# Kernel tuning notes

Hardware: AMD Instinct MI355X
Metric: run time of the kernel (lower is better)

## Reference

```python
import jax, jax.numpy as jnp
import numpy as np

N_NODES = 50000
BN_EPS = 1e-5


def gcn_conv(x, W, b, src, dst, n):
    # PyG GCNConv: add self-loops, symmetric normalization, linear then scatter-add, bias after.
    h = x @ W                                             # [N, out]
    loops = jnp.arange(n, dtype=src.dtype)
    s = jnp.concatenate([src, loops])                     # [E+N]
    d = jnp.concatenate([dst, loops])                     # [E+N]
    deg = jax.ops.segment_sum(jnp.ones_like(d, dtype=h.dtype), d, num_segments=n)
    dinv = jnp.where(deg > 0, jax.lax.rsqrt(deg), 0.0)    # deg^-1/2
    norm = dinv[s] * dinv[d]                              # [E+N]
    msg = h[s] * norm[:, None]                            # gather + scale
    out = jax.ops.segment_sum(msg, d, num_segments=n)     # scatter-add to targets
    return out + b


def batch_norm(x, gamma, beta):
    # training-mode BatchNorm1d: batch stats over node dim, biased variance
    mean = jnp.mean(x, axis=0)
    var = jnp.mean(jnp.square(x - mean), axis=0)
    return (x - mean) * jax.lax.rsqrt(var + BN_EPS) * gamma + beta


def setup_inputs() -> dict:
    key = jax.random.key(0)
    ks = jax.random.split(key, 4)
    n, e = N_NODES, 800000
    c_in, c_hid, c_out = 128, 128, 64
    x = jax.random.normal(ks[0], (n, c_in), dtype=jnp.float32)
    edge_index = jax.random.randint(ks[1], (2, e), 0, n, dtype=jnp.int64)
    W1 = jax.random.normal(ks[2], (c_in, c_hid), dtype=jnp.float32) / np.sqrt(c_in)
    W2 = jax.random.normal(ks[3], (c_hid, c_out), dtype=jnp.float32) / np.sqrt(c_hid)
    return {
        "x": x,
        "edge_index": edge_index,
        "W1": W1,
        "b1": jnp.zeros((c_hid,), jnp.float32),
        "gamma": jnp.ones((c_hid,), jnp.float32),
        "beta": jnp.zeros((c_hid,), jnp.float32),
        "W2": W2,
        "b2": jnp.zeros((c_out,), jnp.float32),
    }


def reference(x, edge_index, W1, b1, gamma, beta, W2, b2):
    src, dst = edge_index[0], edge_index[1]
    n = x.shape[0]
    h = gcn_conv(x, W1, b1, src, dst, n)
    h = batch_norm(h, gamma, beta)
    h = jax.nn.elu(h)
    z = gcn_conv(h, W2, b2, src, dst, n)
    return z
```

## Files before the change

kernel.cpp:

```cpp
#include <hip/hip_runtime.h>
#include <math.h>

#define C_IN 128
#define C_HID 128
#define C_OUT 64
#define BN_EPS 1e-5f

typedef unsigned int uint;
typedef int iv4 __attribute__((ext_vector_type(4)));

__device__ __forceinline__ void fma4(float4& a, float s, const float4& b) {
    a.x += s * b.x; a.y += s * b.y; a.z += s * b.z; a.w += s * b.w;
}
__device__ __forceinline__ uint bfr(float f) {
    uint u = __float_as_uint(f);
    return (u + 0x7fffu + ((u >> 16) & 1u)) >> 16;
}
__device__ __forceinline__ uint pk(float a, float b) { return bfr(a) | (bfr(b) << 16); }
__device__ __forceinline__ float bl(uint u) { return __uint_as_float(u << 16); }
__device__ __forceinline__ float bh(uint u) { return __uint_as_float(u & 0xffff0000u); }

__global__ __launch_bounds__(256) void k_zero(int* __restrict__ deg,
                                              float* __restrict__ gsum,
                                              float* __restrict__ gss, int n) {
    int i = blockIdx.x * 256 + threadIdx.x;
    if (i < n) deg[i] = 0;
    else if (i < n + 128) gsum[i - n] = 0.f;
    else if (i < n + 256) gss[i - n - 128] = 0.f;
}

__global__ void k_deg(const int* __restrict__ dst, int* __restrict__ deg, int E) {
    int e4 = (blockIdx.x * 256 + threadIdx.x) * 4;
    if (e4 + 3 < E) {
        iv4 d4 = __builtin_nontemporal_load((const iv4*)&dst[e4]);
        atomicAdd(&deg[d4.x], 1);
        atomicAdd(&deg[d4.y], 1);
        atomicAdd(&deg[d4.z], 1);
        atomicAdd(&deg[d4.w], 1);
    } else {
        for (int e = e4; e < E; ++e) atomicAdd(&deg[dst[e]], 1);
    }
}

__global__ __launch_bounds__(256) void k_part(const int* __restrict__ deg,
                                              int* __restrict__ part, int n) {
    int i = blockIdx.x * 256 + threadIdx.x;
    int v = (i < n) ? deg[i] : 0;
    #pragma unroll
    for (int o = 32; o > 0; o >>= 1) v += __shfl_down(v, o);
    __shared__ int ls[4];
    if ((threadIdx.x & 63) == 0) ls[threadIdx.x >> 6] = v;
    __syncthreads();
    if (threadIdx.x == 0) part[blockIdx.x] = ls[0] + ls[1] + ls[2] + ls[3];
}

__global__ __launch_bounds__(256) void k_scanp(int* __restrict__ part, int nb) {
    __shared__ int s[256];
    int tid = threadIdx.x;
    int v = (tid < nb) ? part[tid] : 0;
    s[tid] = v;
    __syncthreads();
    for (int o = 1; o < 256; o <<= 1) {
        int t = (tid >= o) ? s[tid - o] : 0;
        __syncthreads();
        s[tid] += t;
        __syncthreads();
    }
    if (tid < nb) part[tid] = s[tid] - v;
}

__global__ __launch_bounds__(256) void k_apply(const int* __restrict__ deg,
                                               const int* __restrict__ part,
                                               int* __restrict__ rowstart,
                                               int* __restrict__ cursor,
                                               float* __restrict__ dinv, int n) {
    int i = blockIdx.x * 256 + threadIdx.x;
    int d = (i < n) ? deg[i] : 0;
    __shared__ int s[256];
    s[threadIdx.x] = d;
    __syncthreads();
    for (int o = 1; o < 256; o <<= 1) {
        int t = (threadIdx.x >= o) ? s[threadIdx.x - o] : 0;
        __syncthreads();
        s[threadIdx.x] += t;
        __syncthreads();
    }
    int incl = s[threadIdx.x];
    int off = part[blockIdx.x];
    if (i < n) {
        rowstart[i] = off + incl - d;
        cursor[i]   = off + incl - d;
        dinv[i] = rsqrtf((float)(d + 1));
        if (i == n - 1) rowstart[n] = off + incl;
    }
}

#define FILL_R 8
#define FILL_CHUNK 4096
__global__ __launch_bounds__(256) void k_fill(const int* __restrict__ src,
                                              const int* __restrict__ dst,
                                              int* __restrict__ cursor,
                                              int* __restrict__ csr,
                                              int E, int rs) {
    int r = blockIdx.x & (FILL_R - 1);
    int c = blockIdx.x >> 3;
    int lo = r * rs, hi = lo + rs;
    int e0 = c * FILL_CHUNK;
    int e1 = e0 + FILL_CHUNK; if (e1 > E) e1 = E;
    for (int e = e0 + threadIdx.x * 4; e + 3 < e1; e += 1024) {
        iv4 d4 = __builtin_nontemporal_load((const iv4*)&dst[e]);
        iv4 s4 = __builtin_nontemporal_load((const iv4*)&src[e]);
        if (d4.x >= lo && d4.x < hi) csr[atomicAdd(&cursor[d4.x], 1)] = s4.x;
        if (d4.y >= lo && d4.y < hi) csr[atomicAdd(&cursor[d4.y], 1)] = s4.y;
        if (d4.z >= lo && d4.z < hi) csr[atomicAdd(&cursor[d4.z], 1)] = s4.z;
        if (d4.w >= lo && d4.w < hi) csr[atomicAdd(&cursor[d4.w], 1)] = s4.w;
    }
    int tail = e1 & ~3;
    if (e1 == E && tail < E) {
        for (int e = tail + threadIdx.x; e < E; e += 256) {
            int d = dst[e];
            if (d >= lo && d < hi) csr[atomicAdd(&cursor[d], 1)] = src[e];
        }
    }
}

__global__ __launch_bounds__(256) void k_gemm1(const float* __restrict__ x,
                                               const float* __restrict__ W,
                                               uint* __restrict__ h, int n) {
    __shared__ float xs[64][68];
    __shared__ float ws[64][68];
    const int tid = threadIdx.x;
    const int cg = tid & 15, rg = tid >> 4;
    const int c0 = cg * 4, r0 = rg * 4;
    const int base = blockIdx.x * 64;
    const int ccol = blockIdx.y * 64;

    float4 acc0 = make_float4(0.f, 0.f, 0.f, 0.f);
    float4 acc1 = acc0, acc2 = acc0, acc3 = acc0;

    for (int p = 0; p < 2; ++p) {
        const int k0 = p * 64;
        if (p) __syncthreads();
        for (int idx = tid; idx < 64 * 16; idx += 256) {
            int row = idx >> 4, c4 = (idx & 15) * 4;
            float4 v = make_float4(0.f, 0.f, 0.f, 0.f);
            if (base + row < n) v = *(const float4*)&x[(size_t)(base + row) * C_IN + k0 + c4];
            *(float4*)&xs[row][c4] = v;
        }
        for (int idx = tid; idx < 64 * 16; idx += 256) {
            int kk = idx >> 4, cc = (idx & 15) * 4;
            *(float4*)&ws[kk][cc] = *(const float4*)&W[(size_t)(k0 + kk) * C_HID + ccol + cc];
        }
        __syncthreads();
        for (int kk = 0; kk < 64; kk += 4) {
            float4 xv0 = *(const float4*)&xs[r0 + 0][kk];
            float4 xv1 = *(const float4*)&xs[r0 + 1][kk];
            float4 xv2 = *(const float4*)&xs[r0 + 2][kk];
            float4 xv3 = *(const float4*)&xs[r0 + 3][kk];
            float4 wv0 = *(const float4*)&ws[kk + 0][c0];
            float4 wv1 = *(const float4*)&ws[kk + 1][c0];
            float4 wv2 = *(const float4*)&ws[kk + 2][c0];
            float4 wv3 = *(const float4*)&ws[kk + 3][c0];
            fma4(acc0, xv0.x, wv0); fma4(acc0, xv0.y, wv1); fma4(acc0, xv0.z, wv2); fma4(acc0, xv0.w, wv3);
            fma4(acc1, xv1.x, wv0); fma4(acc1, xv1.y, wv1); fma4(acc1, xv1.z, wv2); fma4(acc1, xv1.w, wv3);
            fma4(acc2, xv2.x, wv0); fma4(acc2, xv2.y, wv1); fma4(acc2, xv2.z, wv2); fma4(acc2, xv2.w, wv3);
            fma4(acc3, xv3.x, wv0); fma4(acc3, xv3.y, wv1); fma4(acc3, xv3.z, wv2); fma4(acc3, xv3.w, wv3);
        }
    }
    const int cu = (ccol + c0) >> 1;
    if (base + r0 + 0 < n) { uint2 o = make_uint2(pk(acc0.x, acc0.y), pk(acc0.z, acc0.w)); *(uint2*)&h[(size_t)(base + r0 + 0) * 64 + cu] = o; }
    if (base + r0 + 1 < n) { uint2 o = make_uint2(pk(acc1.x, acc1.y), pk(acc1.z, acc1.w)); *(uint2*)&h[(size_t)(base + r0 + 1) * 64 + cu] = o; }
    if (base + r0 + 2 < n) { uint2 o = make_uint2(pk(acc2.x, acc2.y), pk(acc2.z, acc2.w)); *(uint2*)&h[(size_t)(base + r0 + 2) * 64 + cu] = o; }
    if (base + r0 + 3 < n) { uint2 o = make_uint2(pk(acc3.x, acc3.y), pk(acc3.z, acc3.w)); *(uint2*)&h[(size_t)(base + r0 + 3) * 64 + cu] = o; }
}

__global__ __launch_bounds__(256) void k_gather1(const uint2* __restrict__ h,
                                                 const float* __restrict__ dinv,
                                                 const int* __restrict__ rowstart,
                                                 const int* __restrict__ csr,
                                                 const float* __restrict__ b,
                                                 float* __restrict__ out, int n) {
    int wid = (blockIdx.x * 256 + threadIdx.x) >> 6;
    int lane = threadIdx.x & 63;
    int half = lane >> 5, l = lane & 31;
    int v = wid * 2 + half;
    if (v >= n) return;
    float dv = dinv[v];
    int s0 = rowstart[v], s1 = rowstart[v + 1];
    float4 acc;
    {
        uint2 u = h[(size_t)v * 32 + l];
        acc.x = dv * bl(u.x); acc.y = dv * bh(u.x);
        acc.z = dv * bl(u.y); acc.w = dv * bh(u.y);
    }
    int e = s0;
    for (; e + 3 < s1; e += 4) {
        int i0 = csr[e], i1 = csr[e + 1], i2 = csr[e + 2], i3 = csr[e + 3];
        float w0 = dinv[i0], w1 = dinv[i1], w2 = dinv[i2], w3 = dinv[i3];
        uint2 u0 = h[(size_t)i0 * 32 + l];
        uint2 u1 = h[(size_t)i1 * 32 + l];
        uint2 u2 = h[(size_t)i2 * 32 + l];
        uint2 u3 = h[(size_t)i3 * 32 + l];
        acc.x += w0 * bl(u0.x) + w1 * bl(u1.x) + w2 * bl(u2.x) + w3 * bl(u3.x);
        acc.y += w0 * bh(u0.x) + w1 * bh(u1.x) + w2 * bh(u2.x) + w3 * bh(u3.x);
        acc.z += w0 * bl(u0.y) + w1 * bl(u1.y) + w2 * bl(u2.y) + w3 * bl(u3.y);
        acc.w += w0 * bh(u0.y) + w1 * bh(u1.y) + w2 * bh(u2.y) + w3 * bh(u3.y);
    }
    for (; e < s1; ++e) {
        int s = csr[e];
        float w = dinv[s];
        uint2 u = h[(size_t)s * 32 + l];
        acc.x += w * bl(u.x); acc.y += w * bh(u.x);
        acc.z += w * bl(u.y); acc.w += w * bh(u.y);
    }
    float4 bb = *(const float4*)&b[l * 4];
    float4 o;
    o.x = acc.x * dv + bb.x; o.y = acc.y * dv + bb.y;
    o.z = acc.z * dv + bb.z; o.w = acc.w * dv + bb.w;
    *(float4*)&out[(size_t)v * C_HID + l * 4] = o;
}

__global__ __launch_bounds__(256) void k_bnstats(const float* __restrict__ g,
                                                 float* __restrict__ gsum,
                                                 float* __restrict__ gss, int n) {
    float s = 0.f, ss = 0.f;
    int stride = gridDim.x * 256;
    int total = n * C_HID;
    for (int i = blockIdx.x * 256 + threadIdx.x; i < total; i += stride) {
        float v = g[i];
        s += v; ss += v * v;
    }
    __shared__ float ls[256], lss[256];
    ls[threadIdx.x] = s; lss[threadIdx.x] = ss;
    __syncthreads();
    if (threadIdx.x < 128) {
        atomicAdd(&gsum[threadIdx.x], ls[threadIdx.x] + ls[threadIdx.x + 128]);
        atomicAdd(&gss[threadIdx.x], lss[threadIdx.x] + lss[threadIdx.x + 128]);
    }
}

__global__ __launch_bounds__(256) void k_gemm2(const float* __restrict__ g1,
                                               const float* __restrict__ W2,
                                               const float* __restrict__ gsum,
                                               const float* __restrict__ gss,
                                               const float* __restrict__ gamma,
                                               const float* __restrict__ beta,
                                               uint* __restrict__ h2, int n) {
    __shared__ float xs[64][68];
    __shared__ float ws[64][68];
    __shared__ float sc[C_HID], sh[C_HID];
    const int tid = threadIdx.x;
    const int cg = tid & 15, rg = tid >> 4;
    const int c0 = cg * 4, r0 = rg * 4;
    const int base = blockIdx.x * 64;

    if (tid < C_HID) {
        float inv_n = 1.f / (float)n;
        float mean = gsum[tid] * inv_n;
        float var = gss[tid] * inv_n - mean * mean;
        float s = gamma[tid] * rsqrtf(var + BN_EPS);
        sc[tid] = s;
        sh[tid] = beta[tid] - mean * s;
    }
    __syncthreads();

    float4 acc0 = make_float4(0.f, 0.f, 0.f, 0.f);
    float4 acc1 = acc0, acc2 = acc0, acc3 = acc0;

    for (int p = 0; p < 2; ++p) {
        const int k0 = p * 64;
        if (p) __syncthreads();
        for (int idx = tid; idx < 64 * 16; idx += 256) {
            int row = idx >> 4, c4 = (idx & 15) * 4;
            int k = k0 + c4;
            float4 v = make_float4(0.f, 0.f, 0.f, 0.f);
            if (base + row < n) {
                v = *(const float4*)&g1[(size_t)(base + row) * C_HID + k];
                float t;
                t = v.x * sc[k + 0] + sh[k + 0]; v.x = t > 0.f ? t : expm1f(t);
                t = v.y * sc[k + 1] + sh[k + 1]; v.y = t > 0.f ? t : expm1f(t);
                t = v.z * sc[k + 2] + sh[k + 2]; v.z = t > 0.f ? t : expm1f(t);
                t = v.w * sc[k + 3] + sh[k + 3]; v.w = t > 0.f ? t : expm1f(t);
            }
            *(float4*)&xs[row][c4] = v;
        }
        for (int idx = tid; idx < 64 * 16; idx += 256) {
            int kk = idx >> 4, cc = (idx & 15) * 4;
            *(float4*)&ws[kk][cc] = *(const float4*)&W2[(size_t)(k0 + kk) * C_OUT + cc];
        }
        __syncthreads();
        for (int kk = 0; kk < 64; kk += 4) {
            float4 xv0 = *(const float4*)&xs[r0 + 0][kk];
            float4 xv1 = *(const float4*)&xs[r0 + 1][kk];
            float4 xv2 = *(const float4*)&xs[r0 + 2][kk];
            float4 xv3 = *(const float4*)&xs[r0 + 3][kk];
            float4 wv0 = *(const float4*)&ws[kk + 0][c0];
            float4 wv1 = *(const float4*)&ws[kk + 1][c0];
            float4 wv2 = *(const float4*)&ws[kk + 2][c0];
            float4 wv3 = *(const float4*)&ws[kk + 3][c0];
            fma4(acc0, xv0.x, wv0); fma4(acc0, xv0.y, wv1); fma4(acc0, xv0.z, wv2); fma4(acc0, xv0.w, wv3);
            fma4(acc1, xv1.x, wv0); fma4(acc1, xv1.y, wv1); fma4(acc1, xv1.z, wv2); fma4(acc1, xv1.w, wv3);
            fma4(acc2, xv2.x, wv0); fma4(acc2, xv2.y, wv1); fma4(acc2, xv2.z, wv2); fma4(acc2, xv2.w, wv3);
            fma4(acc3, xv3.x, wv0); fma4(acc3, xv3.y, wv1); fma4(acc3, xv3.z, wv2); fma4(acc3, xv3.w, wv3);
        }
    }
    const int cu = c0 >> 1;
    if (base + r0 + 0 < n) { uint2 o = make_uint2(pk(acc0.x, acc0.y), pk(acc0.z, acc0.w)); *(uint2*)&h2[(size_t)(base + r0 + 0) * 32 + cu] = o; }
    if (base + r0 + 1 < n) { uint2 o = make_uint2(pk(acc1.x, acc1.y), pk(acc1.z, acc1.w)); *(uint2*)&h2[(size_t)(base + r0 + 1) * 32 + cu] = o; }
    if (base + r0 + 2 < n) { uint2 o = make_uint2(pk(acc2.x, acc2.y), pk(acc2.z, acc2.w)); *(uint2*)&h2[(size_t)(base + r0 + 2) * 32 + cu] = o; }
    if (base + r0 + 3 < n) { uint2 o = make_uint2(pk(acc3.x, acc3.y), pk(acc3.z, acc3.w)); *(uint2*)&h2[(size_t)(base + r0 + 3) * 32 + cu] = o; }
}

__global__ __launch_bounds__(256) void k_gather2(const uint* __restrict__ h,
                                                 const float* __restrict__ dinv,
                                                 const int* __restrict__ rowstart,
                                                 const int* __restrict__ csr,
                                                 const float* __restrict__ b,
                                                 float* __restrict__ out, int n) {
    int wid = (blockIdx.x * 256 + threadIdx.x) >> 6;
    int lane = threadIdx.x & 63;
    int half = lane >> 5, l = lane & 31;
    int v = wid * 2 + half;
    if (v >= n) return;
    float dv = dinv[v];
    int s0 = rowstart[v], s1 = rowstart[v + 1];
    float2 acc;
    {
        uint u = h[(size_t)v * 32 + l];
        acc.x = dv * bl(u); acc.y = dv * bh(u);
    }
    int e = s0;
    for (; e + 7 < s1; e += 8) {
        int i0 = csr[e], i1 = csr[e + 1], i2 = csr[e + 2], i3 = csr[e + 3];
        int i4 = csr[e + 4], i5 = csr[e + 5], i6 = csr[e + 6], i7 = csr[e + 7];
        float w0 = dinv[i0], w1 = dinv[i1], w2 = dinv[i2], w3 = dinv[i3];
        float w4 = dinv[i4], w5 = dinv[i5], w6 = dinv[i6], w7 = dinv[i7];
        uint u0 = h[(size_t)i0 * 32 + l], u1 = h[(size_t)i1 * 32 + l];
        uint u2 = h[(size_t)i2 * 32 + l], u3 = h[(size_t)i3 * 32 + l];
        uint u4 = h[(size_t)i4 * 32 + l], u5 = h[(size_t)i5 * 32 + l];
        uint u6 = h[(size_t)i6 * 32 + l], u7 = h[(size_t)i7 * 32 + l];
        acc.x += w0 * bl(u0) + w1 * bl(u1) + w2 * bl(u2) + w3 * bl(u3)
               + w4 * bl(u4) + w5 * bl(u5) + w6 * bl(u6) + w7 * bl(u7);
        acc.y += w0 * bh(u0) + w1 * bh(u1) + w2 * bh(u2) + w3 * bh(u3)
               + w4 * bh(u4) + w5 * bh(u5) + w6 * bh(u6) + w7 * bh(u7);
    }
    for (; e < s1; ++e) {
        int s = csr[e];
        float w = dinv[s];
        uint u = h[(size_t)s * 32 + l];
        acc.x += w * bl(u); acc.y += w * bh(u);
    }
    float2 bb = *(const float2*)&b[l * 2];
    float2 o;
    o.x = acc.x * dv + bb.x;
    o.y = acc.y * dv + bb.y;
    *(float2*)&out[(size_t)v * C_OUT + l * 2] = o;
}

extern "C" void kernel_launch(void* const* d_in, const int* in_sizes, int n_in,
                              void* d_out, int out_size, void* d_ws, size_t ws_size,
                              hipStream_t stream) {
    const float* x     = (const float*)d_in[0];
    const int*   ei    = (const int*)d_in[1];
    const float* W1    = (const float*)d_in[2];
    const float* b1    = (const float*)d_in[3];
    const float* gamma = (const float*)d_in[4];
    const float* beta  = (const float*)d_in[5];
    const float* W2    = (const float*)d_in[6];
    const float* b2    = (const float*)d_in[7];
    float* out = (float*)d_out;

    const int n = in_sizes[0] / C_IN;
    const int E = in_sizes[1] / 2;
    const int* src = ei;
    const int* dst = ei + E;

    char* p = (char*)d_ws;
    auto carve = [&](size_t bytes) {
        char* r = p;
        p += (bytes + 255) & ~(size_t)255;
        return r;
    };
    int*   deg      = (int*)  carve((size_t)n * 4);
    int*   rowstart = (int*)  carve((size_t)(n + 1) * 4);
    int*   cursor   = (int*)  carve((size_t)n * 4);
    int*   csr      = (int*)  carve((size_t)E * 4);
    float* dinv     = (float*)carve((size_t)n * 4);
    uint*  h1       = (uint*) carve((size_t)n * 64 * 4);
    float* g1       = (float*)carve((size_t)n * C_HID * 4);
    uint*  h2       = (uint*) carve((size_t)n * 32 * 4);
    float* gsum     = (float*)carve(C_HID * 4);
    float* gss      = (float*)carve(C_HID * 4);
    int*   part     = (int*)  carve(256 * 4);

    const int nb = (n + 255) / 256;
    const int gblocks = (((n + 1) / 2) * 64 + 255) / 256;
    k_zero<<<(n + 256 + 255) / 256, 256, 0, stream>>>(deg, gsum, gss, n);
    k_deg<<<(E / 4 + 255) / 256, 256, 0, stream>>>(dst, deg, E);
    k_gemm1<<<dim3((n + 63) / 64, 2), 256, 0, stream>>>(x, W1, h1, n);
    k_part<<<nb, 256, 0, stream>>>(deg, part, n);
    k_scanp<<<1, 256, 0, stream>>>(part, nb);
    k_apply<<<nb, 256, 0, stream>>>(deg, part, rowstart, cursor, dinv, n);
    int rs = (n + FILL_R - 1) / FILL_R;
    int fc = (E + FILL_CHUNK - 1) / FILL_CHUNK;
    k_fill<<<FILL_R * fc, 256, 0, stream>>>(src, dst, cursor, csr, E, rs);
    k_gather1<<<gblocks, 256, 0, stream>>>((const uint2*)h1, dinv, rowstart, csr, b1, g1, n);
    k_bnstats<<<512, 256, 0, stream>>>(g1, gsum, gss, n);
    k_gemm2<<<(n + 63) / 64, 256, 0, stream>>>(g1, W2, gsum, gss, gamma, beta, h2, n);
    k_gather2<<<gblocks, 256, 0, stream>>>(h2, dinv, rowstart, csr, b2, out, n);
}
```

Baseline: 234.6 us.

## Bucket edges by destination range, store g1 as bf16, widen gather lanes

Result: faster. 219.0 us (-6.7%).

```diff
diff --git a/kernel.cpp b/kernel.cpp
--- a/kernel.cpp
+++ b/kernel.cpp
@@ -5,6 +5,9 @@
 #define C_HID 128
 #define C_OUT 64
 #define BN_EPS 1e-5f
+#define CHUNK 4096
+#define NBB 32
+#define CAP 108192
 
 typedef unsigned int uint;
 typedef int iv4 __attribute__((ext_vector_type(4)));
@@ -22,23 +25,62 @@
 
 __global__ __launch_bounds__(256) void k_zero(int* __restrict__ deg,
                                               float* __restrict__ gsum,
-                                              float* __restrict__ gss, int n) {
+                                              float* __restrict__ gss,
+                                              int* __restrict__ bcur, int n) {
     int i = blockIdx.x * 256 + threadIdx.x;
     if (i < n) deg[i] = 0;
     else if (i < n + 128) gsum[i - n] = 0.f;
     else if (i < n + 256) gss[i - n - 128] = 0.f;
-}
-
-__global__ void k_deg(const int* __restrict__ dst, int* __restrict__ deg, int E) {
-    int e4 = (blockIdx.x * 256 + threadIdx.x) * 4;
-    if (e4 + 3 < E) {
-        iv4 d4 = __builtin_nontemporal_load((const iv4*)&dst[e4]);
-        atomicAdd(&deg[d4.x], 1);
-        atomicAdd(&deg[d4.y], 1);
-        atomicAdd(&deg[d4.z], 1);
-        atomicAdd(&deg[d4.w], 1);
-    } else {
-        for (int e = e4; e < E; ++e) atomicAdd(&deg[dst[e]], 1);
+    else if (i < n + 264) bcur[i - n - 256] = 0;
+}
+
+__global__ __launch_bounds__(256) void k_bucket(const int* __restrict__ src,
+                                                const int* __restrict__ dst,
+                                                int* __restrict__ deg,
+                                                int* __restrict__ bcur,
+                                                int2* __restrict__ stage,
+                                                int E, float binv) {
+    __shared__ int cnt[8], base[8], off[8];
+    if (threadIdx.x < 8) { cnt[threadIdx.x] = 0; off[threadIdx.x] = 0; }
+    __syncthreads();
+    int e0 = blockIdx.x * CHUNK;
+    int e1 = e0 + CHUNK; if (e1 > E) e1 = E;
+    int nv = (e1 - e0) & ~3;
+    for (int e = e0 + threadIdx.x * 4; e < e0 + nv; e += 1024) {
+        iv4 d4 = __builtin_nontemporal_load((const iv4*)&dst[e]);
+        #pragma unroll
+        for (int j = 0; j < 4; ++j) {
+            int d = d4[j];
+            atomicAdd(&deg[d], 1);
+            int b = (int)((float)d * binv); if (b > 7) b = 7;
+            atomicAdd(&cnt[b], 1);
+        }
+    }
+    for (int e = e0 + nv + threadIdx.x; e < e1; e += 256) {
+        int d = dst[e];
+        atomicAdd(&deg[d], 1);
+        int b = (int)((float)d * binv); if (b > 7) b = 7;
+        atomicAdd(&cnt[b], 1);
+    }
+    __syncthreads();
+    if (threadIdx.x < 8) base[threadIdx.x] = atomicAdd(&bcur[threadIdx.x], cnt[threadIdx.x]);
+    __syncthreads();
+    for (int e = e0 + threadIdx.x * 4; e < e0 + nv; e += 1024) {
+        iv4 d4 = *(const iv4*)&dst[e];
+        iv4 s4 = *(const iv4*)&src[e];
+        #pragma unroll
+        for (int j = 0; j < 4; ++j) {
+            int d = d4[j], s = s4[j];
+            int b = (int)((float)d * binv); if (b > 7) b = 7;
+            int o = base[b] + atomicAdd(&off[b], 1);
+            if (o < CAP) stage[(size_t)b * CAP + o] = make_int2(d, s);
+        }
+    }
+    for (int e = e0 + nv + threadIdx.x; e < e1; e += 256) {
+        int d = dst[e], s = src[e];
+        int b = (int)((float)d * binv); if (b > 7) b = 7;
+        int o = base[b] + atomicAdd(&off[b], 1);
+        if (o < CAP) stage[(size_t)b * CAP + o] = make_int2(d, s);
     }
 }
 
@@ -95,32 +137,17 @@
     }
 }
 
-#define FILL_R 8
-#define FILL_CHUNK 4096
-__global__ __launch_bounds__(256) void k_fill(const int* __restrict__ src,
-                                              const int* __restrict__ dst,
-                                              int* __restrict__ cursor,
-                                              int* __restrict__ csr,
-                                              int E, int rs) {
-    int r = blockIdx.x & (FILL_R - 1);
-    int c = blockIdx.x >> 3;
-    int lo = r * rs, hi = lo + rs;
-    int e0 = c * FILL_CHUNK;
-    int e1 = e0 + FILL_CHUNK; if (e1 > E) e1 = E;
-    for (int e = e0 + threadIdx.x * 4; e + 3 < e1; e += 1024) {
-        iv4 d4 = __builtin_nontemporal_load((const iv4*)&dst[e]);
-        iv4 s4 = __builtin_nontemporal_load((const iv4*)&src[e]);
-        if (d4.x >= lo && d4.x < hi) csr[atomicAdd(&cursor[d4.x], 1)] = s4.x;
-        if (d4.y >= lo && d4.y < hi) csr[atomicAdd(&cursor[d4.y], 1)] = s4.y;
-        if (d4.z >= lo && d4.z < hi) csr[atomicAdd(&cursor[d4.z], 1)] = s4.z;
-        if (d4.w >= lo && d4.w < hi) csr[atomicAdd(&cursor[d4.w], 1)] = s4.w;
-    }
-    int tail = e1 & ~3;
-    if (e1 == E && tail < E) {
-        for (int e = tail + threadIdx.x; e < E; e += 256) {
-            int d = dst[e];
-            if (d >= lo && d < hi) csr[atomicAdd(&cursor[d], 1)] = src[e];
-        }
+__global__ __launch_bounds__(256) void k_fill2(const int2* __restrict__ stage,
+                                               const int* __restrict__ bcur,
+                                               int* __restrict__ cursor,
+                                               int* __restrict__ csr) {
+    int b = blockIdx.x & 7;
+    int j = blockIdx.x >> 3;
+    int cnt = bcur[b]; if (cnt > CAP) cnt = CAP;
+    const int2* sp = stage + (size_t)b * CAP;
+    for (int i = j * 256 + threadIdx.x; i < cnt; i += NBB * 256) {
+        int2 pr = sp[i];
+        csr[atomicAdd(&cursor[pr.x], 1)] = pr.y;
     }
 }
 
@@ -174,72 +201,88 @@
     if (base + r0 + 3 < n) { uint2 o = make_uint2(pk(acc3.x, acc3.y), pk(acc3.z, acc3.w)); *(uint2*)&h[(size_t)(base + r0 + 3) * 64 + cu] = o; }
 }
 
-__global__ __launch_bounds__(256) void k_gather1(const uint2* __restrict__ h,
+__global__ __launch_bounds__(256) void k_gather1(const uint4* __restrict__ h,
                                                  const float* __restrict__ dinv,
                                                  const int* __restrict__ rowstart,
                                                  const int* __restrict__ csr,
                                                  const float* __restrict__ b,
-                                                 float* __restrict__ out, int n) {
-    int wid = (blockIdx.x * 256 + threadIdx.x) >> 6;
-    int lane = threadIdx.x & 63;
-    int half = lane >> 5, l = lane & 31;
-    int v = wid * 2 + half;
+                                                 uint4* __restrict__ g1, int n) {
+    int v = (blockIdx.x * 256 + threadIdx.x) >> 4;
+    int l = threadIdx.x & 15;
     if (v >= n) return;
     float dv = dinv[v];
     int s0 = rowstart[v], s1 = rowstart[v + 1];
-    float4 acc;
+    float4 aA, aB;
     {
-        uint2 u = h[(size_t)v * 32 + l];
-        acc.x = dv * bl(u.x); acc.y = dv * bh(u.x);
-        acc.z = dv * bl(u.y); acc.w = dv * bh(u.y);
+        uint4 u = h[(size_t)v * 16 + l];
+        aA.x = dv * bl(u.x); aA.y = dv * bh(u.x); aA.z = dv * bl(u.y); aA.w = dv * bh(u.y);
+        aB.x = dv * bl(u.z); aB.y = dv * bh(u.z); aB.z = dv * bl(u.w); aB.w = dv * bh(u.w);
     }
     int e = s0;
     for (; e + 3 < s1; e += 4) {
         int i0 = csr[e], i1 = csr[e + 1], i2 = csr[e + 2], i3 = csr[e + 3];
         float w0 = dinv[i0], w1 = dinv[i1], w2 = dinv[i2], w3 = dinv[i3];
-        uint2 u0 = h[(size_t)i0 * 32 + l];
-        uint2 u1 = h[(size_t)i1 * 32 + l];
-        uint2 u2 = h[(size_t)i2 * 32 + l];
-        uint2 u3 = h[(size_t)i3 * 32 + l];
-        acc.x += w0 * bl(u0.x) + w1 * bl(u1.x) + w2 * bl(u2.x) + w3 * bl(u3.x);
-        acc.y += w0 * bh(u0.x) + w1 * bh(u1.x) + w2 * bh(u2.x) + w3 * bh(u3.x);
-        acc.z += w0 * bl(u0.y) + w1 * bl(u1.y) + w2 * bl(u2.y) + w3 * bl(u3.y);
-        acc.w += w0 * bh(u0.y) + w1 * bh(u1.y) + w2 * bh(u2.y) + w3 * bh(u3.y);
+        uint4 u0 = h[(size_t)i0 * 16 + l];
+        uint4 u1 = h[(size_t)i1 * 16 + l];
+        uint4 u2 = h[(size_t)i2 * 16 + l];
+        uint4 u3 = h[(size_t)i3 * 16 + l];
+        aA.x += w0 * bl(u0.x) + w1 * bl(u1.x) + w2 * bl(u2.x) + w3 * bl(u3.x);
+        aA.y += w0 * bh(u0.x) + w1 * bh(u1.x) + w2 * bh(u2.x) + w3 * bh(u3.x);
+        aA.z += w0 * bl(u0.y) + w1 * bl(u1.y) + w2 * bl(u2.y) + w3 * bl(u3.y);
+        aA.w += w0 * bh(u0.y) + w1 * bh(u1.y) + w2 * bh(u2.y) + w3 * bh(u3.y);
+        aB.x += w0 * bl(u0.z) + w1 * bl(u1.z) + w2 * bl(u2.z) + w3 * bl(u3.z);
+        aB.y += w0 * bh(u0.z) + w1 * bh(u1.z) + w2 * bh(u2.z) + w3 * bh(u3.z);
+        aB.z += w0 * bl(u0.w) + w1 * bl(u1.w) + w2 * bl(u2.w) + w3 * bl(u3.w);
+        aB.w += w0 * bh(u0.w) + w1 * bh(u1.w) + w2 * bh(u2.w) + w3 * bh(u3.w);
     }
     for (; e < s1; ++e) {
         int s = csr[e];
         float w = dinv[s];
-        uint2 u = h[(size_t)s * 32 + l];
-        acc.x += w * bl(u.x); acc.y += w * bh(u.x);
-        acc.z += w * bl(u.y); acc.w += w * bh(u.y);
-    }
-    float4 bb = *(const float4*)&b[l * 4];
-    float4 o;
-    o.x = acc.x * dv + bb.x; o.y = acc.y * dv + bb.y;
-    o.z = acc.z * dv + bb.z; o.w = acc.w * dv + bb.w;
-    *(float4*)&out[(size_t)v * C_HID + l * 4] = o;
-}
-
-__global__ __launch_bounds__(256) void k_bnstats(const float* __restrict__ g,
+        uint4 u = h[(size_t)s * 16 + l];
+        aA.x += w * bl(u.x); aA.y += w * bh(u.x); aA.z += w * bl(u.y); aA.w += w * bh(u.y);
+        aB.x += w * bl(u.z); aB.y += w * bh(u.z); aB.z += w * bl(u.w); aB.w += w * bh(u.w);
+    }
+    float4 b0 = *(const float4*)&b[l * 8];
+    float4 b1v = *(const float4*)&b[l * 8 + 4];
+    uint4 o;
+    o.x = pk(aA.x * dv + b0.x,  aA.y * dv + b0.y);
+    o.y = pk(aA.z * dv + b0.z,  aA.w * dv + b0.w);
+    o.z = pk(aB.x * dv + b1v.x, aB.y * dv + b1v.y);
+    o.w = pk(aB.z * dv + b1v.z, aB.w * dv + b1v.w);
+    g1[(size_t)v * 16 + l] = o;
+}
+
+__global__ __launch_bounds__(256) void k_bnstats(const uint4* __restrict__ g,
                                                  float* __restrict__ gsum,
                                                  float* __restrict__ gss, int n) {
-    float s = 0.f, ss = 0.f;
+    float4 sA = make_float4(0.f,0.f,0.f,0.f), sB = sA, qA = sA, qB = sA;
+    int total = n * 16;
     int stride = gridDim.x * 256;
-    int total = n * C_HID;
     for (int i = blockIdx.x * 256 + threadIdx.x; i < total; i += stride) {
-        float v = g[i];
-        s += v; ss += v * v;
-    }
-    __shared__ float ls[256], lss[256];
-    ls[threadIdx.x] = s; lss[threadIdx.x] = ss;
+        uint4 u = g[i];
+        float v0 = bl(u.x), v1 = bh(u.x), v2 = bl(u.y), v3 = bh(u.y);
+        float v4 = bl(u.z), v5 = bh(u.z), v6 = bl(u.w), v7 = bh(u.w);
+        sA.x += v0; sA.y += v1; sA.z += v2; sA.w += v3;
+        sB.x += v4; sB.y += v5; sB.z += v6; sB.w += v7;
+        qA.x += v0*v0; qA.y += v1*v1; qA.z += v2*v2; qA.w += v3*v3;
+        qB.x += v4*v4; qB.y += v5*v5; qB.z += v6*v6; qB.w += v7*v7;
+    }
+    __shared__ float sb[128], qb[128];
+    if (threadIdx.x < 128) { sb[threadIdx.x] = 0.f; qb[threadIdx.x] = 0.f; }
+    __syncthreads();
+    int c0 = (threadIdx.x & 15) * 8;
+    atomicAdd(&sb[c0+0], sA.x); atomicAdd(&sb[c0+1], sA.y); atomicAdd(&sb[c0+2], sA.z); atomicAdd(&sb[c0+3], sA.w);
+    atomicAdd(&sb[c0+4], sB.x); atomicAdd(&sb[c0+5], sB.y); atomicAdd(&sb[c0+6], sB.z); atomicAdd(&sb[c0+7], sB.w);
+    atomicAdd(&qb[c0+0], qA.x); atomicAdd(&qb[c0+1], qA.y); atomicAdd(&qb[c0+2], qA.z); atomicAdd(&qb[c0+3], qA.w);
+    atomicAdd(&qb[c0+4], qB.x); atomicAdd(&qb[c0+5], qB.y); atomicAdd(&qb[c0+6], qB.z); atomicAdd(&qb[c0+7], qB.w);
     __syncthreads();
     if (threadIdx.x < 128) {
-        atomicAdd(&gsum[threadIdx.x], ls[threadIdx.x] + ls[threadIdx.x + 128]);
-        atomicAdd(&gss[threadIdx.x], lss[threadIdx.x] + lss[threadIdx.x + 128]);
-    }
-}
-
-__global__ __launch_bounds__(256) void k_gemm2(const float* __restrict__ g1,
+        atomicAdd(&gsum[threadIdx.x], sb[threadIdx.x]);
+        atomicAdd(&gss[threadIdx.x], qb[threadIdx.x]);
+    }
+}
+
+__global__ __launch_bounds__(256) void k_gemm2(const uint4* __restrict__ g1,
                                                const float* __restrict__ W2,
                                                const float* __restrict__ gsum,
                                                const float* __restrict__ gss,
@@ -270,19 +313,24 @@
     for (int p = 0; p < 2; ++p) {
         const int k0 = p * 64;
         if (p) __syncthreads();
-        for (int idx = tid; idx < 64 * 16; idx += 256) {
-            int row = idx >> 4, c4 = (idx & 15) * 4;
-            int k = k0 + c4;
-            float4 v = make_float4(0.f, 0.f, 0.f, 0.f);
+        for (int idx = tid; idx < 64 * 8; idx += 256) {
+            int row = idx >> 3, q4 = idx & 7;
+            int k = k0 + q4 * 8;
+            float4 vA = make_float4(0.f,0.f,0.f,0.f), vB = vA;
             if (base + row < n) {
-                v = *(const float4*)&g1[(size_t)(base + row) * C_HID + k];
+                uint4 u = g1[(size_t)(base + row) * 16 + (k >> 3)];
                 float t;
-                t = v.x * sc[k + 0] + sh[k + 0]; v.x = t > 0.f ? t : expm1f(t);
-                t = v.y * sc[k + 1] + sh[k + 1]; v.y = t > 0.f ? t : expm1f(t);
-                t = v.z * sc[k + 2] + sh[k + 2]; v.z = t > 0.f ? t : expm1f(t);
-                t = v.w * sc[k + 3] + sh[k + 3]; v.w = t > 0.f ? t : expm1f(t);
+                t = bl(u.x) * sc[k+0] + sh[k+0]; vA.x = t > 0.f ? t : expm1f(t);
+                t = bh(u.x) * sc[k+1] + sh[k+1]; vA.y = t > 0.f ? t : expm1f(t);
+                t = bl(u.y) * sc[k+2] + sh[k+2]; vA.z = t > 0.f ? t : expm1f(t);
+                t = bh(u.y) * sc[k+3] + sh[k+3]; vA.w = t > 0.f ? t : expm1f(t);
+                t = bl(u.z) * sc[k+4] + sh[k+4]; vB.x = t > 0.f ? t : expm1f(t);
+                t = bh(u.z) * sc[k+5] + sh[k+5]; vB.y = t > 0.f ? t : expm1f(t);
+                t = bl(u.w) * sc[k+6] + sh[k+6]; vB.z = t > 0.f ? t : expm1f(t);
+                t = bh(u.w) * sc[k+7] + sh[k+7]; vB.w = t > 0.f ? t : expm1f(t);
             }
-            *(float4*)&xs[row][c4] = v;
+            *(float4*)&xs[row][q4 * 8] = vA;
+            *(float4*)&xs[row][q4 * 8 + 4] = vB;
         }
         for (int idx = tid; idx < 64 * 16; idx += 256) {
             int kk = idx >> 4, cc = (idx & 15) * 4;
@@ -311,50 +359,46 @@
     if (base + r0 + 3 < n) { uint2 o = make_uint2(pk(acc3.x, acc3.y), pk(acc3.z, acc3.w)); *(uint2*)&h2[(size_t)(base + r0 + 3) * 32 + cu] = o; }
 }
 
-__global__ __launch_bounds__(256) void k_gather2(const uint* __restrict__ h,
+__global__ __launch_bounds__(256) void k_gather2(const uint2* __restrict__ h,
                                                  const float* __restrict__ dinv,
                                                  const int* __restrict__ rowstart,
                                                  const int* __restrict__ csr,
                                                  const float* __restrict__ b,
                                                  float* __restrict__ out, int n) {
-    int wid = (blockIdx.x * 256 + threadIdx.x) >> 6;
-    int lane = threadIdx.x & 63;
-    int half = lane >> 5, l = lane & 31;
-    int v = wid * 2 + half;
+    int v = (blockIdx.x * 256 + threadIdx.x) >> 4;
+    int l = threadIdx.x & 15;
     if (v >= n) return;
     float dv = dinv[v];
     int s0 = rowstart[v], s1 = rowstart[v + 1];
-    float2 acc;
+    float4 a;
     {
-        uint u = h[(size_t)v * 32 + l];
-        acc.x = dv * bl(u); acc.y = dv * bh(u);
+        uint2 u = h[(size_t)v * 16 + l];
+        a.x = dv * bl(u.x); a.y = dv * bh(u.x); a.z = dv * bl(u.y); a.w = dv * bh(u.y);
     }
     int e = s0;
-    for (; e + 7 < s1; e += 8) {
+    for (; e + 3 < s1; e += 4) {
         int i0 = csr[e], i1 = csr[e + 1], i2 = csr[e + 2], i3 = csr[e + 3];
-        int i4 = csr[e + 4], i5 = csr[e + 5], i6 = csr[e + 6], i7 = csr[e + 7];
         float w0 = dinv[i0], w1 = dinv[i1], w2 = dinv[i2], w3 = dinv[i3];
-        float w4 = dinv[i4], w5 = dinv[i5], w6 = dinv[i6], w7 = dinv[i7];
-        uint u0 = h[(size_t)i0 * 32 + l], u1 = h[(size_t)i1 * 32 + l];
-        uint u2 = h[(size_t)i2 * 32 + l], u3 = h[(size_t)i3 * 32 + l];
-        uint u4 = h[(size_t)i4 * 32 + l], u5 = h[(size_t)i5 * 32 + l];
-        uint u6 = h[(size_t)i6 * 32 + l], u7 = h[(size_t)i7 * 32 + l];
-        acc.x += w0 * bl(u0) + w1 * bl(u1) + w2 * bl(u2) + w3 * bl(u3)
-               + w4 * bl(u4) + w5 * bl(u5) + w6 * bl(u6) + w7 * bl(u7);
-        acc.y += w0 * bh(u0) + w1 * bh(u1) + w2 * bh(u2) + w3 * bh(u3)
-               + w4 * bh(u4) + w5 * bh(u5) + w6 * bh(u6) + w7 * bh(u7);
+        uint2 u0 = h[(size_t)i0 * 16 + l];
+        uint2 u1 = h[(size_t)i1 * 16 + l];
+        uint2 u2 = h[(size_t)i2 * 16 + l];
+        uint2 u3 = h[(size_t)i3 * 16 + l];
+        a.x += w0 * bl(u0.x) + w1 * bl(u1.x) + w2 * bl(u2.x) + w3 * bl(u3.x);
+        a.y += w0 * bh(u0.x) + w1 * bh(u1.x) + w2 * bh(u2.x) + w3 * bh(u3.x);
+        a.z += w0 * bl(u0.y) + w1 * bl(u1.y) + w2 * bl(u2.y) + w3 * bl(u3.y);
+        a.w += w0 * bh(u0.y) + w1 * bh(u1.y) + w2 * bh(u2.y) + w3 * bh(u3.y);
     }
     for (; e < s1; ++e) {
         int s = csr[e];
         float w = dinv[s];
-        uint u = h[(size_t)s * 32 + l];
-        acc.x += w * bl(u); acc.y += w * bh(u);
-    }
-    float2 bb = *(const float2*)&b[l * 2];
-    float2 o;
-    o.x = acc.x * dv + bb.x;
-    o.y = acc.y * dv + bb.y;
-    *(float2*)&out[(size_t)v * C_OUT + l * 2] = o;
+        uint2 u = h[(size_t)s * 16 + l];
+        a.x += w * bl(u.x); a.y += w * bh(u.x); a.z += w * bl(u.y); a.w += w * bh(u.y);
+    }
+    float4 bb = *(const float4*)&b[l * 4];
+    float4 o;
+    o.x = a.x * dv + bb.x; o.y = a.y * dv + bb.y;
+    o.z = a.z * dv + bb.z; o.w = a.w * dv + bb.w;
+    *(float4*)&out[(size_t)v * C_OUT + l * 4] = o;
 }
 
 extern "C" void kernel_launch(void* const* d_in, const int* in_sizes, int n_in,
@@ -387,25 +431,28 @@
     int*   csr      = (int*)  carve((size_t)E * 4);
     float* dinv     = (float*)carve((size_t)n * 4);
     uint*  h1       = (uint*) carve((size_t)n * 64 * 4);
-    float* g1       = (float*)carve((size_t)n * C_HID * 4);
+    uint*  g1       = (uint*) carve((size_t)n * 64 * 4);
     uint*  h2       = (uint*) carve((size_t)n * 32 * 4);
     float* gsum     = (float*)carve(C_HID * 4);
     float* gss      = (float*)carve(C_HID * 4);
     int*   part     = (int*)  carve(256 * 4);
+    int*   bcur     = (int*)  carve(8 * 4);
+    int2*  stage    = (int2*) carve((size_t)8 * CAP * 8);
 
     const int nb = (n + 255) / 256;
-    const int gblocks = (((n + 1) / 2) * 64 + 255) / 256;
-    k_zero<<<(n + 256 + 255) / 256, 256, 0, stream>>>(deg, gsum, gss, n);
-    k_deg<<<(E / 4 + 255) / 256, 256, 0, stream>>>(dst, deg, E);
+    const int gblocks = (n * 16 + 255) / 256;
+    const int fc = (E + CHUNK - 1) / CHUNK;
+    const float binv = 8.0f / (float)n;
+
+    k_zero<<<(n + 264 + 255) / 256, 256, 0, stream>>>(deg, gsum, gss, bcur, n);
+    k_bucket<<<fc, 256, 0, stream>>>(src, dst, deg, bcur, stage, E, binv);
     k_gemm1<<<dim3((n + 63) / 64, 2), 256, 0, stream>>>(x, W1, h1, n);
     k_part<<<nb, 256, 0, stream>>>(deg, part, n);
     k_scanp<<<1, 256, 0, stream>>>(part, nb);
     k_apply<<<nb, 256, 0, stream>>>(deg, part, rowstart, cursor, dinv, n);
-    int rs = (n + FILL_R - 1) / FILL_R;
-    int fc = (E + FILL_CHUNK - 1) / FILL_CHUNK;
-    k_fill<<<FILL_R * fc, 256, 0, stream>>>(src, dst, cursor, csr, E, rs);
-    k_gather1<<<gblocks, 256, 0, stream>>>((const uint2*)h1, dinv, rowstart, csr, b1, g1, n);
-    k_bnstats<<<512, 256, 0, stream>>>(g1, gsum, gss, n);
-    k_gemm2<<<(n + 63) / 64, 256, 0, stream>>>(g1, W2, gsum, gss, gamma, beta, h2, n);
-    k_gather2<<<gblocks, 256, 0, stream>>>(h2, dinv, rowstart, csr, b2, out, n);
-}
+    k_fill2<<<8 * NBB, 256, 0, stream>>>(stage, bcur, cursor, csr);
+    k_gather1<<<gblocks, 256, 0, stream>>>((const uint4*)h1, dinv, rowstart, csr, b1, (uint4*)g1, n);
+    k_bnstats<<<512, 256, 0, stream>>>((const uint4*)g1, gsum, gss, n);
+    k_gemm2<<<(n + 63) / 64, 256, 0, stream>>>((const uint4*)g1, W2, gsum, gss, gamma, beta, h2, n);
+    k_gather2<<<gblocks, 256, 0, stream>>>((const uint2*)h2, dinv, rowstart, csr, b2, out, n);
+}
```
